# Optimization experiments

Measured on AMD Instinct MI355X. Metric: run time of the kernel, lower is better.

Reference implementation:

```python
import jax, jax.numpy as jnp
import numpy as np
from jax import lax

GRID = 16
NUM_UNITS = 10
N_UNITS = NUM_UNITS * 2
UNIT_OBS_SIZE = 32
GRID_OBS_SIZE = GRID * GRID + N_UNITS * 10 + 2  # 458
OBS_SIZE = GRID_OBS_SIZE + UNIT_OBS_SIZE        # 490
ACTION_SIZE = 16
B = 16384
CNN_FEATURES = 256
UNIT_FEATURES = 64
TRUNK_FEATURES = 256


def setup_inputs() -> dict:
    key = jax.random.key(0)
    ks = jax.random.split(key, 24)
    obs = jax.random.uniform(ks[0], (B, OBS_SIZE), dtype=jnp.float32)
    # Distinct cell per unit per sample -> scatter-add == serial set semantics.
    n_cells = (GRID - 1) * (GRID - 1)
    cells = jnp.argsort(jax.random.uniform(ks[1], (B, n_cells)), axis=-1)[:, :N_UNITS]
    r = (cells // (GRID - 1)).astype(jnp.float32) / (GRID - 1)
    c = (cells % (GRID - 1)).astype(jnp.float32) / (GRID - 1)
    base = GRID * GRID
    uidx = jnp.arange(N_UNITS)
    obs = obs.at[:, base + uidx * 10 + 2].set(r).at[:, base + uidx * 10 + 3].set(c)

    def w(k, shape, s=0.1):
        return jax.random.normal(k, shape, dtype=jnp.float32) * s

    return {
        "obs": obs,
        "conv1_w": w(ks[2], (32, 9, 3, 3)), "conv1_b": jnp.zeros((32,), jnp.float32),
        "conv2_w": w(ks[3], (64, 32, 3, 3)), "conv2_b": jnp.zeros((64,), jnp.float32),
        "conv3_w": w(ks[4], (64, 64, 3, 3)), "conv3_b": jnp.zeros((64,), jnp.float32),
        "fc_w": w(ks[5], (CNN_FEATURES, 64 * 4 * 4)), "fc_b": jnp.zeros((CNN_FEATURES,), jnp.float32),
        "u1_w": w(ks[6], (64, UNIT_OBS_SIZE)), "u1_b": jnp.zeros((64,), jnp.float32),
        "u2_w": w(ks[7], (UNIT_FEATURES, 64)), "u2_b": jnp.zeros((UNIT_FEATURES,), jnp.float32),
        "t1_w": w(ks[8], (TRUNK_FEATURES, CNN_FEATURES + UNIT_FEATURES)), "t1_b": jnp.zeros((TRUNK_FEATURES,), jnp.float32),
        "t2_w": w(ks[9], (TRUNK_FEATURES, TRUNK_FEATURES)), "t2_b": jnp.zeros((TRUNK_FEATURES,), jnp.float32),
        "actor_w": w(ks[10], (ACTION_SIZE, TRUNK_FEATURES), 0.01), "actor_b": jnp.zeros((ACTION_SIZE,), jnp.float32),
        "critic_w": w(ks[11], (1, TRUNK_FEATURES)), "critic_b": jnp.zeros((1,), jnp.float32),
    }


def _preprocess(obs):
    Bn = obs.shape[0]
    terrain = obs[:, :GRID * GRID].reshape(Bn, 1, GRID, GRID)
    units = obs[:, GRID * GRID:GRID * GRID + N_UNITS * 10].reshape(Bn, N_UNITS, 10)
    unit_obs = obs[:, GRID_OBS_SIZE:]
    team = units[..., 1]
    r = (units[..., 2] * (GRID - 1)).astype(jnp.int32)
    c = (units[..., 3] * (GRID - 1)).astype(jnp.int32)
    hp = units[..., 4]
    moved = units[..., 5]
    acted = units[..., 6]
    alive = hp > 0
    blue = team < 0.5
    flat = r * GRID + c                       # (B, N_UNITS)
    bidx = jnp.arange(Bn)[:, None]

    def scat(vals, mask):
        z = jnp.zeros((Bn, GRID * GRID), obs.dtype)
        z = z.at[bidx, flat].add(jnp.where(mask, vals, 0.0))
        return z.reshape(Bn, 1, GRID, GRID)

    ones = jnp.ones_like(hp)
    mb = alive & blue
    mr = alive & ~blue
    grid = jnp.concatenate([
        terrain,
        scat(ones, mb), scat(ones, mr),
        scat(hp, mb), scat(hp, mr),
        scat(moved, mb), scat(acted, mb),
        scat(moved, mr), scat(acted, mr),
    ], axis=1)                                # (B, 9, 16, 16)
    return grid, unit_obs


def _conv(x, w, b):
    y = lax.conv_general_dilated(x, w, (1, 1), 'SAME',
                                 dimension_numbers=('NCHW', 'OIHW', 'NCHW'))
    return jax.nn.relu(y + b[None, :, None, None])


def _lin(x, w, b):
    return x @ w.T + b


def reference(obs, conv1_w, conv1_b, conv2_w, conv2_b, conv3_w, conv3_b,
              fc_w, fc_b, u1_w, u1_b, u2_w, u2_b, t1_w, t1_b, t2_w, t2_b,
              actor_w, actor_b, critic_w, critic_b):
    grid, unit = _preprocess(obs)
    x = _conv(grid, conv1_w, conv1_b)
    x = _conv(x, conv2_w, conv2_b)
    x = _conv(x, conv3_w, conv3_b)            # (B, 64, 16, 16)
    # AdaptiveAvgPool2d((4,4)) on 16x16 == 4x4 mean pooling
    Bn = x.shape[0]
    x = x.reshape(Bn, 64, 4, 4, 4, 4).mean(axis=(3, 5))
    x = x.reshape(Bn, 64 * 4 * 4)
    cnn_feat = jax.nn.relu(_lin(x, fc_w, fc_b))
    uh = jax.nn.relu(_lin(unit, u1_w, u1_b))
    unit_feat = jax.nn.relu(_lin(uh, u2_w, u2_b))
    t = jnp.concatenate([cnn_feat, unit_feat], axis=-1)
    t = jax.nn.relu(_lin(t, t1_w, t1_b))
    t = jax.nn.relu(_lin(t, t2_w, t2_b))
    logits = _lin(t, actor_w, actor_b)        # (B, ACTION_SIZE)
    value = _lin(t, critic_w, critic_b)       # (B, 1)
    return logits, value
```

## Files before the change

### kernel.cpp

```cpp
#include <hip/hip_runtime.h>

#define OBS_STRIDE 490

typedef _Float16 half8 __attribute__((ext_vector_type(8)));
typedef _Float16 half4 __attribute__((ext_vector_type(4)));
typedef float f32x4 __attribute__((ext_vector_type(4)));

union H8 { half8 h; uint4 u; };

#define FC_BASE 126
#define T1_BASE 638
#define T2_BASE 798
#define HD_BASE 926
#define NFRAG   942

__global__ __launch_bounds__(256) void prep_weights(
    const float* __restrict__ w1, const float* __restrict__ w2,
    const float* __restrict__ w3,
    const float* __restrict__ fcw, const float* __restrict__ t1w,
    const float* __restrict__ t2w,
    const float* __restrict__ aw,  const float* __restrict__ cw,
    uint4* __restrict__ wfrag)
{
    int gid = blockIdx.x * 256 + threadIdx.x;
    if (gid >= NFRAG * 64) return;
    int fid = gid >> 6, lane = gid & 63;
    H8 v;
    if (fid < 126) {
        const float* W; int C, sh, kt, mt;
        if (fid < 18)      { int f = fid;      W = w1; C = 9;  sh = f >> 1; kt = 0;            mt = f & 1; }
        else if (fid < 54) { int f = fid - 18; W = w2; C = 32; sh = f >> 2; kt = 0;            mt = f & 3; }
        else               { int f = fid - 54; W = w3; C = 64; sh = f >> 3; kt = (f >> 2) & 1; mt = f & 3; }
        int o  = mt * 16 + (lane & 15);
        int c0 = kt * 32 + ((lane >> 4) << 3);
        #pragma unroll
        for (int i = 0; i < 8; ++i) {
            int c = c0 + i;
            v.h[i] = (c < C) ? (_Float16)W[(o * C + c) * 9 + sh] : (_Float16)0.f;
        }
    } else {
        int o16 = lane & 15, k0 = (lane >> 4) << 3;
        if (fid < HD_BASE) {
            const float* W; int K, f;
            if (fid < T1_BASE)      { f = fid - FC_BASE; W = fcw; K = 1024; }
            else if (fid < T2_BASE) { f = fid - T1_BASE; W = t1w; K = 320;  }
            else                    { f = fid - T2_BASE; W = t2w; K = 256;  }
            int ks = f >> 4, mtg = f & 15;
            int o = mtg * 16 + o16;
            int kb = ks * 32 + k0;
            #pragma unroll
            for (int i = 0; i < 8; ++i)
                v.h[i] = (_Float16)W[(size_t)o * K + kb + i];
        } else {
            int f = fid - HD_BASE;
            int ks = f >> 1, mtg = f & 1;
            int kb = ks * 32 + k0;
            #pragma unroll
            for (int i = 0; i < 8; ++i) {
                float x;
                if (mtg == 0)      x = aw[o16 * 256 + kb + i];
                else if (o16 == 0) x = cw[kb + i];
                else               x = 0.f;
                v.h[i] = (_Float16)x;
            }
        }
    }
    wfrag[gid] = v.u;
}

template<int KT, int MT, int FRAG_BASE>
__device__ __forceinline__ void conv_layer(
    unsigned char* Abuf, const uint4* __restrict__ wfrag,
    const float* __restrict__ bias, int lane, int wv)
{
    const int x = lane & 15;
    const int q = lane >> 4;
    f32x4 acc[4][MT];
    #pragma unroll
    for (int mt = 0; mt < MT; ++mt) {
        f32x4 bv = *(const f32x4*)(bias + mt * 16 + q * 4);
        #pragma unroll
        for (int row = 0; row < 4; ++row) acc[row][mt] = bv;
    }
    #pragma unroll
    for (int sh = 0; sh < 9; ++sh) {
        const int dy = sh / 3 - 1, dx = sh % 3 - 1;
        const int xs = x + dx + 1;
        #pragma unroll
        for (int kt = 0; kt < KT; ++kt) {
            H8 wf[MT];
            #pragma unroll
            for (int mt = 0; mt < MT; ++mt)
                wf[mt].u = wfrag[(FRAG_BASE + (sh * KT + kt) * MT + mt) * 64 + lane];
            const int chunk = ((kt * 4 + q) ^ (xs & 7)) << 4;
            #pragma unroll
            for (int row = 0; row < 4; ++row) {
                const int ys = wv * 4 + row + dy + 1;
                half8 bf = *(const half8*)(Abuf + ys * 2304 + xs * 128 + chunk);
                #pragma unroll
                for (int mt = 0; mt < MT; ++mt)
                    acc[row][mt] = __builtin_amdgcn_mfma_f32_16x16x32_f16(
                        wf[mt].h, bf, acc[row][mt], 0, 0, 0);
            }
        }
    }
    __syncthreads();
    const int xs1 = x + 1;
    #pragma unroll
    for (int row = 0; row < 4; ++row) {
        const int ys = wv * 4 + row + 1;
        #pragma unroll
        for (int mt = 0; mt < MT; ++mt) {
            half4 hv;
            #pragma unroll
            for (int r = 0; r < 4; ++r) hv[r] = (_Float16)fmaxf(acc[row][mt][r], 0.f);
            const int ob = mt * 32 + q * 8;
            const int addr = ys * 2304 + xs1 * 128 + ((((ob >> 4) ^ (xs1 & 7))) << 4) + (ob & 15);
            *(half4*)(Abuf + addr) = hv;
        }
    }
    __syncthreads();
}

__global__ __launch_bounds__(256, 2) void conv_kernel(
    const float* __restrict__ obs,
    const uint4* __restrict__ wfrag,
    const float* __restrict__ b1, const float* __restrict__ b2,
    const float* __restrict__ b3,
    _Float16* __restrict__ pooled)
{
    __shared__ alignas(16) unsigned char Abuf[18 * 18 * 128];
    __shared__ float G[8][256];

    const int tid = threadIdx.x;
    const int b = blockIdx.x;
    const float* ob = obs + (size_t)b * OBS_STRIDE;

    {
        uint4 z = {0, 0, 0, 0};
        uint4* A4 = (uint4*)Abuf;
        for (int i = tid; i < 2592; i += 256) A4[i] = z;
        float4 zf = {0.f, 0.f, 0.f, 0.f};
        float4* G4 = (float4*)G;
        for (int i = tid; i < 512; i += 256) G4[i] = zf;
    }
    __syncthreads();

    if (tid < 20) {
        const float* up = ob + 256 + tid * 10;
        float team = up[1], rf = up[2], cf = up[3];
        float hp = up[4], mv = up[5], ac = up[6];
        if (hp > 0.f) {
            int r = (int)(rf * 15.f), c = (int)(cf * 15.f);
            int flat = r * 16 + c;
            if (team < 0.5f) {
                atomicAdd(&G[0][flat], 1.f);
                atomicAdd(&G[2][flat], hp);
                atomicAdd(&G[4][flat], mv);
                atomicAdd(&G[5][flat], ac);
            } else {
                atomicAdd(&G[1][flat], 1.f);
                atomicAdd(&G[3][flat], hp);
                atomicAdd(&G[6][flat], mv);
                atomicAdd(&G[7][flat], ac);
            }
        }
    }
    __syncthreads();

    {
        int p = tid & 255, xsg = (p & 15) + 1, ysg = (p >> 4) + 1;
        H8 v;
        v.h[0] = (_Float16)ob[p];
        #pragma unroll
        for (int c = 1; c < 8; ++c) v.h[c] = (_Float16)G[c - 1][p];
        *(uint4*)(Abuf + ysg * 2304 + xsg * 128 + ((xsg & 7) << 4)) = v.u;
        *(_Float16*)(Abuf + ysg * 2304 + xsg * 128 + ((1 ^ (xsg & 7)) << 4)) = (_Float16)G[7][p];
    }
    __syncthreads();

    const int lane = tid & 63, wv = tid >> 6;
    conv_layer<1, 2, 0 >(Abuf, wfrag, b1, lane, wv);
    conv_layer<1, 4, 18>(Abuf, wfrag, b2, lane, wv);
    conv_layer<2, 4, 54>(Abuf, wfrag, b3, lane, wv);

    {
        int qq = tid & 15, cg = tid >> 4;
        int ph = qq >> 2, pw = qq & 3;
        int ch0 = cg * 4;
        float s[4] = {0.f, 0.f, 0.f, 0.f};
        int ob2 = ch0 * 2;
        #pragma unroll
        for (int dy = 0; dy < 4; ++dy) {
            int ys = ph * 4 + dy + 1;
            #pragma unroll
            for (int dx = 0; dx < 4; ++dx) {
                int xs = pw * 4 + dx + 1;
                int addr = ys * 2304 + xs * 128 + ((((ob2 >> 4) ^ (xs & 7))) << 4) + (ob2 & 15);
                half4 hv = *(const half4*)(Abuf + addr);
                #pragma unroll
                for (int cc = 0; cc < 4; ++cc) s[cc] += (float)hv[cc];
            }
        }
        _Float16* pb = pooled + (size_t)b * 1024;
        #pragma unroll
        for (int cc = 0; cc < 4; ++cc)
            pb[(ch0 + cc) * 16 + qq] = (_Float16)(s[cc] * 0.0625f);
    }
}

__global__ __launch_bounds__(256) void tail_kernel(
    const float* __restrict__ obs,
    const _Float16* __restrict__ pooled,
    const uint4* __restrict__ wfrag,
    const float* __restrict__ fcb,
    const float* __restrict__ u1w, const float* __restrict__ u1b,
    const float* __restrict__ u2w, const float* __restrict__ u2b,
    const float* __restrict__ t1b, const float* __restrict__ t2b,
    const float* __restrict__ ab,  const float* __restrict__ cb,
    float* __restrict__ out, int NB)
{
    __shared__ alignas(16) _Float16 tcT[32][344];
    __shared__ alignas(16) _Float16 uh[32][72];

    const int tid  = threadIdx.x;
    const int lane = tid & 63, w = tid >> 6;
    const int nl   = lane & 15, q = lane >> 4;
    const int r0   = blockIdx.x * 32;

    {
        const int r = tid >> 3, t8 = tid & 7;
        const float* up = obs + (size_t)(r0 + r) * OBS_STRIDE + 458;
        float xin[32];
        #pragma unroll
        for (int k2 = 0; k2 < 16; ++k2) {
            float2 v = *(const float2*)(up + k2 * 2);
            xin[k2 * 2] = v.x; xin[k2 * 2 + 1] = v.y;
        }
        #pragma unroll
        for (int oo = 0; oo < 8; ++oo) {
            int o = t8 * 8 + oo;
            float a = u1b[o];
            const float* wr = u1w + o * 32;
            #pragma unroll
            for (int k = 0; k < 32; ++k) a = fmaf(xin[k], wr[k], a);
            uh[r][o] = (_Float16)fmaxf(a, 0.f);
        }
    }
    __syncthreads();

    {
        const int r = tid >> 3, t8 = tid & 7;
        float xin[64];
        #pragma unroll
        for (int k8 = 0; k8 < 8; ++k8) {
            half8 v = *(const half8*)&uh[r][k8 * 8];
            #pragma unroll
            for (int j = 0; j < 8; ++j) xin[k8 * 8 + j] = (float)v[j];
        }
        #pragma unroll
        for (int oo = 0; oo < 8; ++oo) {
            int o = t8 * 8 + oo;
            float a = u2b[o];
            const float* wr = u2w + o * 64;
            #pragma unroll
            for (int k = 0; k < 64; ++k) a = fmaf(xin[k], wr[k], a);
            tcT[r][256 + o] = (_Float16)fmaxf(a, 0.f);
        }
    }

    {
        f32x4 acc[4][2];
        #pragma unroll
        for (int mt = 0; mt < 4; ++mt) {
            f32x4 bv = *(const f32x4*)(fcb + (w * 4 + mt) * 16 + q * 4);
            acc[mt][0] = bv; acc[mt][1] = bv;
        }
        for (int ks = 0; ks < 32; ++ks) {
            H8 bf[2];
            #pragma unroll
            for (int g = 0; g < 2; ++g)
                bf[g].u = *(const uint4*)(pooled + (size_t)(r0 + g * 16 + nl) * 1024 + ks * 32 + q * 8);
            #pragma unroll
            for (int mt = 0; mt < 4; ++mt) {
                H8 af; af.u = wfrag[(size_t)(FC_BASE + ks * 16 + w * 4 + mt) * 64 + lane];
                #pragma unroll
                for (int g = 0; g < 2; ++g)
                    acc[mt][g] = __builtin_amdgcn_mfma_f32_16x16x32_f16(af.h, bf[g].h, acc[mt][g], 0, 0, 0);
            }
        }
        #pragma unroll
        for (int mt = 0; mt < 4; ++mt)
            #pragma unroll
            for (int g = 0; g < 2; ++g) {
                half4 hv;
                #pragma unroll
                for (int r = 0; r < 4; ++r) hv[r] = (_Float16)fmaxf(acc[mt][g][r], 0.f);
                *(half4*)&tcT[g * 16 + nl][(w * 4 + mt) * 16 + q * 4] = hv;
            }
    }
    __syncthreads();

    {
        f32x4 acc[4][2];
        #pragma unroll
        for (int mt = 0; mt < 4; ++mt) {
            f32x4 bv = *(const f32x4*)(t1b + (w * 4 + mt) * 16 + q * 4);
            acc[mt][0] = bv; acc[mt][1] = bv;
        }
        for (int ks = 0; ks < 10; ++ks) {
            H8 bf[2];
            #pragma unroll
            for (int g = 0; g < 2; ++g)
                bf[g].h = *(const half8*)&tcT[g * 16 + nl][ks * 32 + q * 8];
            #pragma unroll
            for (int mt = 0; mt < 4; ++mt) {
                H8 af; af.u = wfrag[(size_t)(T1_BASE + ks * 16 + w * 4 + mt) * 64 + lane];
                #pragma unroll
                for (int g = 0; g < 2; ++g)
                    acc[mt][g] = __builtin_amdgcn_mfma_f32_16x16x32_f16(af.h, bf[g].h, acc[mt][g], 0, 0, 0);
            }
        }
        __syncthreads();
        #pragma unroll
        for (int mt = 0; mt < 4; ++mt)
            #pragma unroll
            for (int g = 0; g < 2; ++g) {
                half4 hv;
                #pragma unroll
                for (int r = 0; r < 4; ++r) hv[r] = (_Float16)fmaxf(acc[mt][g][r], 0.f);
                *(half4*)&tcT[g * 16 + nl][(w * 4 + mt) * 16 + q * 4] = hv;
            }
    }
    __syncthreads();

    {
        f32x4 acc[4][2];
        #pragma unroll
        for (int mt = 0; mt < 4; ++mt) {
            f32x4 bv = *(const f32x4*)(t2b + (w * 4 + mt) * 16 + q * 4);
            acc[mt][0] = bv; acc[mt][1] = bv;
        }
        for (int ks = 0; ks < 8; ++ks) {
            H8 bf[2];
            #pragma unroll
            for (int g = 0; g < 2; ++g)
                bf[g].h = *(const half8*)&tcT[g * 16 + nl][ks * 32 + q * 8];
            #pragma unroll
            for (int mt = 0; mt < 4; ++mt) {
                H8 af; af.u = wfrag[(size_t)(T2_BASE + ks * 16 + w * 4 + mt) * 64 + lane];
                #pragma unroll
                for (int g = 0; g < 2; ++g)
                    acc[mt][g] = __builtin_amdgcn_mfma_f32_16x16x32_f16(af.h, bf[g].h, acc[mt][g], 0, 0, 0);
            }
        }
        __syncthreads();
        #pragma unroll
        for (int mt = 0; mt < 4; ++mt)
            #pragma unroll
            for (int g = 0; g < 2; ++g) {
                half4 hv;
                #pragma unroll
                for (int r = 0; r < 4; ++r) hv[r] = (_Float16)fmaxf(acc[mt][g][r], 0.f);
                *(half4*)&tcT[g * 16 + nl][(w * 4 + mt) * 16 + q * 4] = hv;
            }
    }
    __syncthreads();

    if (w < 2) {
        f32x4 acc[2];
        if (w == 0) {
            f32x4 bv = *(const f32x4*)(ab + q * 4);
            acc[0] = bv; acc[1] = bv;
        } else {
            f32x4 bv = {0.f, 0.f, 0.f, 0.f};
            if (q == 0) bv[0] = cb[0];
            acc[0] = bv; acc[1] = bv;
        }
        for (int ks = 0; ks < 8; ++ks) {
            H8 af; af.u = wfrag[(size_t)(HD_BASE + ks * 2 + w) * 64 + lane];
            #pragma unroll
            for (int g = 0; g < 2; ++g) {
                half8 bf = *(const half8*)&tcT[g * 16 + nl][ks * 32 + q * 8];
                acc[g] = __builtin_amdgcn_mfma_f32_16x16x32_f16(af.h, bf, acc[g], 0, 0, 0);
            }
        }
        if (w == 0) {
            #pragma unroll
            for (int g = 0; g < 2; ++g) {
                float4 o4 = {acc[g][0], acc[g][1], acc[g][2], acc[g][3]};
                *(float4*)(out + (size_t)(r0 + g * 16 + nl) * 16 + q * 4) = o4;
            }
        } else if (q == 0) {
            #pragma unroll
            for (int g = 0; g < 2; ++g)
                out[(size_t)NB * 16 + r0 + g * 16 + nl] = acc[g][0];
        }
    }
}

extern "C" void kernel_launch(void* const* d_in, const int* in_sizes, int n_in,
                              void* d_out, int out_size, void* d_ws, size_t ws_size,
                              hipStream_t stream)
{
    const float* obs = (const float*)d_in[0];
    const float* w1  = (const float*)d_in[1];
    const float* b1  = (const float*)d_in[2];
    const float* w2  = (const float*)d_in[3];
    const float* b2  = (const float*)d_in[4];
    const float* w3  = (const float*)d_in[5];
    const float* b3  = (const float*)d_in[6];
    const float* fcw = (const float*)d_in[7];
    const float* fcb = (const float*)d_in[8];
    const float* u1w = (const float*)d_in[9];
    const float* u1b = (const float*)d_in[10];
    const float* u2w = (const float*)d_in[11];
    const float* u2b = (const float*)d_in[12];
    const float* t1w = (const float*)d_in[13];
    const float* t1b = (const float*)d_in[14];
    const float* t2w = (const float*)d_in[15];
    const float* t2b = (const float*)d_in[16];
    const float* aw  = (const float*)d_in[17];
    const float* ab  = (const float*)d_in[18];
    const float* cw  = (const float*)d_in[19];
    const float* cb  = (const float*)d_in[20];

    const int NB = in_sizes[0] / OBS_STRIDE;
    _Float16* pooled = (_Float16*)d_ws;
    uint4* wfrag = (uint4*)((char*)d_ws + (size_t)NB * 1024 * 2);

    prep_weights<<<(NFRAG * 64 + 255) / 256, 256, 0, stream>>>(
        w1, w2, w3, fcw, t1w, t2w, aw, cw, wfrag);
    conv_kernel<<<NB, 256, 0, stream>>>(obs, (const uint4*)wfrag, b1, b2, b3, pooled);
    tail_kernel<<<NB / 32, 256, 0, stream>>>(obs, pooled, (const uint4*)wfrag,
                                             fcb, u1w, u1b, u2w, u2b,
                                             t1b, t2b, ab, cb,
                                             (float*)d_out, NB);
}
```

Baseline: 550.4 us.

## Drop vertical halo rows and G scratch to shrink LDS and double occupancy

```diff
diff --git a/kernel.cpp b/kernel.cpp
--- a/kernel.cpp
+++ b/kernel.cpp
@@ -96,11 +96,13 @@
             #pragma unroll
             for (int row = 0; row < 4; ++row) {
                 const int ys = wv * 4 + row + dy + 1;
-                half8 bf = *(const half8*)(Abuf + ys * 2304 + xs * 128 + chunk);
-                #pragma unroll
-                for (int mt = 0; mt < MT; ++mt)
-                    acc[row][mt] = __builtin_amdgcn_mfma_f32_16x16x32_f16(
-                        wf[mt].h, bf, acc[row][mt], 0, 0, 0);
+                if (ys >= 1 && ys <= 16) {
+                    half8 bf = *(const half8*)(Abuf + (ys - 1) * 2304 + xs * 128 + chunk);
+                    #pragma unroll
+                    for (int mt = 0; mt < MT; ++mt)
+                        acc[row][mt] = __builtin_amdgcn_mfma_f32_16x16x32_f16(
+                            wf[mt].h, bf, acc[row][mt], 0, 0, 0);
+                }
             }
         }
     }
@@ -108,41 +110,52 @@
     const int xs1 = x + 1;
     #pragma unroll
     for (int row = 0; row < 4; ++row) {
-        const int ys = wv * 4 + row + 1;
+        const int yi = wv * 4 + row;
         #pragma unroll
         for (int mt = 0; mt < MT; ++mt) {
             half4 hv;
             #pragma unroll
             for (int r = 0; r < 4; ++r) hv[r] = (_Float16)fmaxf(acc[row][mt][r], 0.f);
             const int ob = mt * 32 + q * 8;
-            const int addr = ys * 2304 + xs1 * 128 + ((((ob >> 4) ^ (xs1 & 7))) << 4) + (ob & 15);
+            const int addr = yi * 2304 + xs1 * 128 + ((((ob >> 4) ^ (xs1 & 7))) << 4) + (ob & 15);
             *(half4*)(Abuf + addr) = hv;
         }
     }
     __syncthreads();
 }
 
-__global__ __launch_bounds__(256, 2) void conv_kernel(
+__global__ __launch_bounds__(256, 4) void conv_kernel(
     const float* __restrict__ obs,
     const uint4* __restrict__ wfrag,
     const float* __restrict__ b1, const float* __restrict__ b2,
     const float* __restrict__ b3,
     _Float16* __restrict__ pooled)
 {
-    __shared__ alignas(16) unsigned char Abuf[18 * 18 * 128];
-    __shared__ float G[8][256];
+    __shared__ alignas(16) unsigned char Abuf[16 * 18 * 128];
 
     const int tid = threadIdx.x;
     const int b = blockIdx.x;
     const float* ob = obs + (size_t)b * OBS_STRIDE;
 
     {
-        uint4 z = {0, 0, 0, 0};
         uint4* A4 = (uint4*)Abuf;
-        for (int i = tid; i < 2592; i += 256) A4[i] = z;
-        float4 zf = {0.f, 0.f, 0.f, 0.f};
-        float4* G4 = (float4*)G;
-        for (int i = tid; i < 512; i += 256) G4[i] = zf;
+        #pragma unroll
+        for (int it = 0; it < 9; ++it) {
+            int i = tid + it * 256;
+            int r0 = i / 144;
+            int rem = i - r0 * 144;
+            int xs = rem >> 3, pc = rem & 7;
+            int c = pc ^ (xs & 7);
+            uint4 v = {0, 0, 0, 0};
+            if (c == 0 && xs >= 1 && xs <= 16) {
+                H8 h;
+                #pragma unroll
+                for (int j = 0; j < 8; ++j) h.h[j] = (_Float16)0.f;
+                h.h[0] = (_Float16)ob[r0 * 16 + xs - 1];
+                v = h.u;
+            }
+            A4[i] = v;
+        }
     }
     __syncthreads();
 
@@ -152,30 +165,18 @@
         float hp = up[4], mv = up[5], ac = up[6];
         if (hp > 0.f) {
             int r = (int)(rf * 15.f), c = (int)(cf * 15.f);
-            int flat = r * 16 + c;
+            const unsigned base = (unsigned)(r * 2304 + (c + 1) * 128);
+            const int sw = (c + 1) & 7;
+#define SCAT_W(CH, VAL) { const int obyte = (CH) * 2;                                   \
+        *(_Float16*)(Abuf + base + ((((obyte >> 4) ^ sw)) << 4) + (obyte & 15)) =       \
+            (_Float16)(VAL); }
             if (team < 0.5f) {
-                atomicAdd(&G[0][flat], 1.f);
-                atomicAdd(&G[2][flat], hp);
-                atomicAdd(&G[4][flat], mv);
-                atomicAdd(&G[5][flat], ac);
+                SCAT_W(1, 1.f) SCAT_W(3, hp) SCAT_W(5, mv) SCAT_W(6, ac)
             } else {
-                atomicAdd(&G[1][flat], 1.f);
-                atomicAdd(&G[3][flat], hp);
-                atomicAdd(&G[6][flat], mv);
-                atomicAdd(&G[7][flat], ac);
-            }
-        }
-    }
-    __syncthreads();
-
-    {
-        int p = tid & 255, xsg = (p & 15) + 1, ysg = (p >> 4) + 1;
-        H8 v;
-        v.h[0] = (_Float16)ob[p];
-        #pragma unroll
-        for (int c = 1; c < 8; ++c) v.h[c] = (_Float16)G[c - 1][p];
-        *(uint4*)(Abuf + ysg * 2304 + xsg * 128 + ((xsg & 7) << 4)) = v.u;
-        *(_Float16*)(Abuf + ysg * 2304 + xsg * 128 + ((1 ^ (xsg & 7)) << 4)) = (_Float16)G[7][p];
+                SCAT_W(2, 1.f) SCAT_W(4, hp) SCAT_W(7, mv) SCAT_W(8, ac)
+            }
+#undef SCAT_W
+        }
     }
     __syncthreads();
 
@@ -192,11 +193,11 @@
         int ob2 = ch0 * 2;
         #pragma unroll
         for (int dy = 0; dy < 4; ++dy) {
-            int ys = ph * 4 + dy + 1;
+            int yi = ph * 4 + dy;
             #pragma unroll
             for (int dx = 0; dx < 4; ++dx) {
                 int xs = pw * 4 + dx + 1;
-                int addr = ys * 2304 + xs * 128 + ((((ob2 >> 4) ^ (xs & 7))) << 4) + (ob2 & 15);
+                int addr = yi * 2304 + xs * 128 + ((((ob2 >> 4) ^ (xs & 7))) << 4) + (ob2 & 15);
                 half4 hv = *(const half4*)(Abuf + addr);
                 #pragma unroll
                 for (int cc = 0; cc < 4; ++cc) s[cc] += (float)hv[cc];
```

After: 565.0 us. 2.7% more time.
